# Optimization experiments

Measured on AMD Instinct MI355X. Metric: run time of the kernel, lower is better.

Reference implementation:

```python
import math
import jax, jax.numpy as jnp
import numpy as np

B, T, D, S = 4, 8192, 1024, 32  # batch, seq, dim, num_slots; segment L = T // S


def setup_inputs() -> dict:
    key = jax.random.key(0)
    ks = jax.random.split(key, 11)
    d_inv_sqrt = D ** -0.5
    return {
        "x": jax.random.normal(ks[0], (B, T, D), jnp.float32),
        "gate_w": jax.random.normal(ks[1], (D, D), jnp.float32) * d_inv_sqrt,
        "gate_b": jnp.zeros((D,), jnp.float32),
        "read_q_w": jax.random.normal(ks[2], (D, D), jnp.float32) * 0.02,
        "read_k_w": jax.random.normal(ks[3], (D, D), jnp.float32) * 0.02,
        "read_v_w": jax.random.normal(ks[4], (D, D), jnp.float32) * 0.02,
        "output_w": jax.random.normal(ks[5], (D, D), jnp.float32) * d_inv_sqrt,
        "memory_slots": jax.random.normal(ks[6], (S, D), jnp.float32) * 0.02,
        "write_q_w": jax.random.normal(ks[7], (D, D), jnp.float32) * 0.02,
        "write_k_w": jax.random.normal(ks[8], (D, D), jnp.float32) * 0.02,
        "write_v_w": jax.random.normal(ks[9], (D, D), jnp.float32) * 0.02,
    }


def reference(x, gate_w, gate_b, read_q_w, read_k_w, read_v_w, output_w,
              memory_slots, write_q_w, write_k_w, write_v_w):
    b, t, d = x.shape
    s = memory_slots.shape[0]
    L = t // s  # segment length
    scale = 1.0 / math.sqrt(d)

    h = x @ gate_w.T + gate_b  # [B,T,D] gate pre-activation

    # --- write: per-slot attention over that slot's segment (block-diagonal) ---
    q = memory_slots @ write_q_w.T                      # [S,D]
    xs = x.reshape(b, s, L, d)                          # [B,S,L,D]
    k = xs @ write_k_w.T                                # [B,S,L,D]
    v = xs @ write_v_w.T                                # [B,S,L,D]
    wqk = jnp.einsum('sd,bsld->bsl', q, k) * scale      # [B,S,L]
    wattn = jax.nn.softmax(wqk, axis=-1)
    memory = jnp.einsum('bsl,bsld->bsd', wattn, v)      # [B,S,D]

    # --- read: masked cross-attention from tokens to memory slots ---
    rq = x @ read_q_w.T                                 # [B,T,D]
    rk = memory @ read_k_w.T                            # [B,S,D]
    rv = memory @ read_v_w.T                            # [B,S,D]
    rqk = jnp.einsum('btd,bsd->bts', rq, rk) * scale    # [B,T,S]
    seg = jnp.arange(t) // L                            # token -> segment index
    mask = seg[:, None] <= jnp.arange(s)[None, :]       # [T,S]; attend to slots >= own segment
    rqk = jnp.where(mask[None, :, :], rqk, -jnp.inf)
    rattn = jax.nn.softmax(rqk, axis=-1)
    read = jnp.einsum('bts,bsd->btd', rattn, rv)        # [B,T,D]

    y = x + jax.nn.sigmoid(h) * read
    out = y @ output_w.T
    return out, memory
```

## Files before the change

### kernel.cpp

```cpp
#include <hip/hip_runtime.h>
#include <stdint.h>

#define TB 4
#define TT 8192
#define TD 1024
#define TS 32
#define TL 256
#define BT 32768

typedef unsigned short u16;
typedef __bf16 bf16x8 __attribute__((ext_vector_type(8)));
typedef float f32x4 __attribute__((ext_vector_type(4)));

typedef uint32_t u32_g __attribute__((address_space(1)));
typedef uint32_t u32_l __attribute__((address_space(3)));

#define VMWAIT(N) asm volatile("s_waitcnt vmcnt(" #N ")" ::: "memory")
#define LGKM0()   asm volatile("s_waitcnt lgkmcnt(0)" ::: "memory")

__device__ __forceinline__ u16 f2b(float f){
  union { float f; uint32_t u; } a; a.f = f;
  uint32_t r = a.u + 0x7FFFu + ((a.u >> 16) & 1u);
  return (u16)(r >> 16);
}
__device__ __forceinline__ float b2f(u16 u){
  union { uint32_t u; float f; } a; a.u = ((uint32_t)u) << 16;
  return a.f;
}
__device__ __forceinline__ void gll16(const void* g, void* l){
  __builtin_amdgcn_global_load_lds((const u32_g*)g, (u32_l*)l, 16, 0, 0);
}

__global__ void k_tran(const float* __restrict__ w0, const float* __restrict__ w1,
                       const float* __restrict__ w2, const float* __restrict__ w3,
                       const float* __restrict__ w4, const float* __restrict__ ms,
                       u16* __restrict__ t0, u16* __restrict__ t1,
                       u16* __restrict__ t2, u16* __restrict__ t3,
                       u16* __restrict__ t4, u16* __restrict__ msb){
  int tid = threadIdx.x, z = blockIdx.z;
  if (z == 5){
    int i = (blockIdx.y*16 + blockIdx.x)*256 + tid;
    if (i < 8192){
      float4 v = ((const float4*)ms)[i];
      ushort4 u; u.x=f2b(v.x); u.y=f2b(v.y); u.z=f2b(v.z); u.w=f2b(v.w);
      ((ushort4*)msb)[i] = u;
    }
    return;
  }
  const float* src = (z==0)?w0:(z==1)?w1:(z==2)?w2:(z==3)?w3:w4;
  u16* dst = (z==0)?t0:(z==1)?t1:(z==2)?t2:(z==3)?t3:t4;
  __shared__ float sT[64][65];
  int r0 = blockIdx.y*64, c0 = blockIdx.x*64;
  int lr = tid >> 2, lc = (tid & 3)*16;
  #pragma unroll
  for (int j=0; j<4; ++j){
    float4 v = *(const float4*)(src + (size_t)(r0+lr)*TD + c0 + lc + j*4);
    sT[lr][lc+j*4+0]=v.x; sT[lr][lc+j*4+1]=v.y; sT[lr][lc+j*4+2]=v.z; sT[lr][lc+j*4+3]=v.w;
  }
  __syncthreads();
  int oc = tid >> 2, orh = (tid & 3)*16;
  #pragma unroll
  for (int j=0; j<4; ++j){
    ushort4 u;
    u.x = f2b(sT[orh+j*4+0][oc]);
    u.y = f2b(sT[orh+j*4+1][oc]);
    u.z = f2b(sT[orh+j*4+2][oc]);
    u.w = f2b(sT[orh+j*4+3][oc]);
    *(ushort4*)(dst + (size_t)(c0+oc)*TD + r0 + orh + j*4) = u;
  }
}

__global__ __launch_bounds__(512) void k_smmw(
    const u16* __restrict__ A0, const u16* __restrict__ W0, u16* __restrict__ O0, int tr0, float s0,
    const u16* __restrict__ A1, const u16* __restrict__ W1, u16* __restrict__ O1, int tr1, float s1){
  const u16 *A, *W; u16* O; int tr; float sc;
  if (blockIdx.z == 0){ A=A0; W=W0; O=O0; tr=tr0; sc=s0; }
  else                { A=A1; W=W1; O=O1; tr=tr1; sc=s1; }
  int tid = threadIdx.x, lane = tid & 63, wv = tid >> 6;
  int r15 = lane & 15, kg = lane >> 4;
  int wr = wv >> 2, wc = wv & 3;
  int m0 = blockIdx.y*128 + wr*64;
  int n0 = blockIdx.x*128 + wc*32;
  const u16* ap = A + (size_t)(m0 + r15)*TD + kg*8;
  const u16* bp = W + (size_t)(n0 + r15)*TD + kg*8;
  f32x4 acc[4][2];
  #pragma unroll
  for (int i=0;i<4;i++){ f32x4 z={0,0,0,0}; acc[i][0]=z; acc[i][1]=z; }
  #pragma unroll 2
  for (int k0=0; k0<TD; k0+=32){
    bf16x8 b0 = *(const bf16x8*)(bp + k0);
    bf16x8 b1 = *(const bf16x8*)(bp + 16*TD + k0);
    bf16x8 a0 = *(const bf16x8*)(ap + k0);
    bf16x8 a1 = *(const bf16x8*)(ap + 16*TD + k0);
    bf16x8 a2 = *(const bf16x8*)(ap + 32*TD + k0);
    bf16x8 a3 = *(const bf16x8*)(ap + 48*TD + k0);
    acc[0][0] = __builtin_amdgcn_mfma_f32_16x16x32_bf16(a0, b0, acc[0][0], 0,0,0);
    acc[0][1] = __builtin_amdgcn_mfma_f32_16x16x32_bf16(a0, b1, acc[0][1], 0,0,0);
    acc[1][0] = __builtin_amdgcn_mfma_f32_16x16x32_bf16(a1, b0, acc[1][0], 0,0,0);
    acc[1][1] = __builtin_amdgcn_mfma_f32_16x16x32_bf16(a1, b1, acc[1][1], 0,0,0);
    acc[2][0] = __builtin_amdgcn_mfma_f32_16x16x32_bf16(a2, b0, acc[2][0], 0,0,0);
    acc[2][1] = __builtin_amdgcn_mfma_f32_16x16x32_bf16(a2, b1, acc[2][1], 0,0,0);
    acc[3][0] = __builtin_amdgcn_mfma_f32_16x16x32_bf16(a3, b0, acc[3][0], 0,0,0);
    acc[3][1] = __builtin_amdgcn_mfma_f32_16x16x32_bf16(a3, b1, acc[3][1], 0,0,0);
  }
  #pragma unroll
  for (int mf=0; mf<4; ++mf){
    #pragma unroll
    for (int nf=0; nf<2; ++nf){
      int n = n0 + nf*16 + r15;
      #pragma unroll
      for (int qq=0; qq<4; ++qq){
        float v = acc[mf][nf][qq]*sc;
        int m = m0 + mf*16 + kg*4 + qq;
        if (tr) O[(size_t)n*TD + m] = f2b(v);
        else    O[(size_t)m*TD + n] = f2b(v);
      }
    }
  }
}

__global__ __launch_bounds__(512) void k_qk32(const u16* __restrict__ msb, const u16* __restrict__ WzT,
                                              float* __restrict__ qkp){
  int tid = threadIdx.x, lane = tid & 63, wv = tid >> 6;
  int r15 = lane & 15, kg = lane >> 4;
  int n0 = blockIdx.x*128 + wv*16;
  int kbase = blockIdx.y*512;
  const u16* ap = msb + (size_t)r15*TD + kbase + kg*8;
  const u16* bp = WzT + (size_t)(n0 + r15)*TD + kbase + kg*8;
  f32x4 a0 = {0,0,0,0}, a1 = {0,0,0,0};
  #pragma unroll 4
  for (int k0=0; k0<512; k0+=32){
    bf16x8 b  = *(const bf16x8*)(bp + k0);
    bf16x8 x0 = *(const bf16x8*)(ap + k0);
    bf16x8 x1 = *(const bf16x8*)(ap + 16*TD + k0);
    a0 = __builtin_amdgcn_mfma_f32_16x16x32_bf16(x0, b, a0, 0,0,0);
    a1 = __builtin_amdgcn_mfma_f32_16x16x32_bf16(x1, b, a1, 0,0,0);
  }
  const float sc = 1.0f/32.0f;
  float* o = qkp + (size_t)blockIdx.y*32768;
  #pragma unroll
  for (int qq=0; qq<4; ++qq){
    o[(size_t)(kg*4 + qq)*TD + n0 + r15]      = a0[qq]*sc;
    o[(size_t)(16 + kg*4 + qq)*TD + n0 + r15] = a1[qq]*sc;
  }
}

__global__ void k_convdot(const float* __restrict__ x, const float* __restrict__ qkp,
                          u16* __restrict__ xb, float* __restrict__ wqk,
                          const float* __restrict__ s0, const float* __restrict__ s1,
                          const float* __restrict__ s2, const float* __restrict__ s3,
                          const float* __restrict__ s4,
                          u16* __restrict__ d0, u16* __restrict__ d1,
                          u16* __restrict__ d2, u16* __restrict__ d3,
                          u16* __restrict__ d4){
  int tid = threadIdx.x;
  if (blockIdx.x >= 2048){
    int i = (blockIdx.x - 2048)*256 + tid;
    int mi = i >> 18, j = i & 262143;
    const float* src; u16* dst;
    if      (mi == 0){ src = s0; dst = d0; }
    else if (mi == 1){ src = s1; dst = d1; }
    else if (mi == 2){ src = s2; dst = d2; }
    else if (mi == 3){ src = s3; dst = d3; }
    else             { src = s4; dst = d4; }
    float4 v = ((const float4*)src)[j];
    ushort4 u; u.x=f2b(v.x); u.y=f2b(v.y); u.z=f2b(v.z); u.w=f2b(v.w);
    ((ushort4*)dst)[j] = u;
    return;
  }
  int lane = tid & 63, wv = tid >> 6;
  long bt0 = (long)blockIdx.x * 16;
  int sseg = (int)((bt0 & (TT-1)) >> 8);
  float qv[16];
  #pragma unroll
  for (int i=0;i<4;i++){
    const float* qp = qkp + (size_t)sseg*TD + i*256 + lane*4;
    float4 ta = *(const float4*)qp;
    float4 tb = *(const float4*)(qp + 32768);
    qv[i*4+0]=ta.x+tb.x; qv[i*4+1]=ta.y+tb.y; qv[i*4+2]=ta.z+tb.z; qv[i*4+3]=ta.w+tb.w;
  }
  for (int tok = wv; tok < 16; tok += 4){
    long bt = bt0 + tok;
    const float* xr = x + bt*TD;
    float dot = 0.f;
    #pragma unroll
    for (int i=0;i<4;i++){
      float4 t = *(const float4*)(xr + i*256 + lane*4);
      ushort4 u; u.x=f2b(t.x); u.y=f2b(t.y); u.z=f2b(t.z); u.w=f2b(t.w);
      *(ushort4*)(xb + bt*TD + i*256 + lane*4) = u;
      dot += t.x*qv[i*4] + t.y*qv[i*4+1] + t.z*qv[i*4+2] + t.w*qv[i*4+3];
    }
    #pragma unroll
    for (int o=32;o;o>>=1) dot += __shfl_xor(dot, o);
    if (lane == 0) wqk[bt] = dot;
  }
}

__global__ void k_wattn(const float* __restrict__ wqk, const u16* __restrict__ xb,
                        u16* __restrict__ xbarb){
  __shared__ float sw[TL];
  __shared__ float red[8];
  __shared__ f32x4 part[4][64];
  int tid = threadIdx.x, lane = tid & 63, wv = tid >> 6;
  int b = blockIdx.x >> 5, s = blockIdx.x & 31;
  long base = (long)b*TT + (long)s*TL;
  float v = wqk[base + tid];
  float m = v;
  #pragma unroll
  for (int o=32;o;o>>=1) m = fmaxf(m, __shfl_xor(m, o));
  if (lane == 0) red[wv] = m;
  __syncthreads();
  m = fmaxf(fmaxf(red[0], red[1]), fmaxf(red[2], red[3]));
  float e = __expf(v - m);
  float sm = e;
  #pragma unroll
  for (int o=32;o;o>>=1) sm += __shfl_xor(sm, o);
  if (lane == 0) red[4+wv] = sm;
  __syncthreads();
  sm = red[4]+red[5]+red[6]+red[7];
  sw[tid] = e / sm;
  __syncthreads();
  int d = blockIdx.y*256 + lane*4;
  const u16* xp = xb + (base + wv*64)*TD + d;
  f32x4 acc = {0,0,0,0};
  #pragma unroll 8
  for (int i=0; i<64; ++i){
    float w = sw[wv*64 + i];
    ushort4 u = *(const ushort4*)(xp + (size_t)i*TD);
    acc[0] += w*b2f(u.x); acc[1] += w*b2f(u.y); acc[2] += w*b2f(u.z); acc[3] += w*b2f(u.w);
  }
  part[wv][lane] = acc;
  __syncthreads();
  if (wv == 0){
    f32x4 t0 = part[0][lane], t1 = part[1][lane], t2 = part[2][lane], t3 = part[3][lane];
    ushort4 o;
    o.x = f2b(t0[0]+t1[0]+t2[0]+t3[0]);
    o.y = f2b(t0[1]+t1[1]+t2[1]+t3[1]);
    o.z = f2b(t0[2]+t1[2]+t2[2]+t3[2]);
    o.w = f2b(t0[3]+t1[3]+t2[3]+t3[3]);
    *(ushort4*)(xbarb + ((size_t)b*TS + s)*TD + d) = o;
  }
}

__global__ __launch_bounds__(512) void k_xbar3(const u16* __restrict__ xbarb,
                                               const u16* __restrict__ Wv, const u16* __restrict__ WdT,
                                               const u16* __restrict__ We,
                                               float* __restrict__ memo, u16* __restrict__ rkb,
                                               u16* __restrict__ rvT){
  int z = blockIdx.z;
  const u16* W = (z==0) ? Wv : (z==1) ? WdT : We;
  int tid = threadIdx.x, lane = tid & 63, wv = tid >> 6;
  int r15 = lane & 15, kg = lane >> 4;
  int wr = wv >> 2, wc = wv & 3;
  int n0 = blockIdx.x*128 + wc*32;
  const u16* ap = xbarb + (size_t)(wr*64 + r15)*TD + kg*8;
  const u16* bp = W + (size_t)(n0 + r15)*TD + kg*8;
  f32x4 acc[4][2];
  #pragma unroll
  for (int i=0;i<4;i++){ f32x4 zz={0,0,0,0}; acc[i][0]=zz; acc[i][1]=zz; }
  #pragma unroll 2
  for (int k0=0; k0<TD; k0+=32){
    bf16x8 b0 = *(const bf16x8*)(bp + k0);
    bf16x8 b1 = *(const bf16x8*)(bp + 16*TD + k0);
    bf16x8 a0 = *(const bf16x8*)(ap + k0);
    bf16x8 a1 = *(const bf16x8*)(ap + 16*TD + k0);
    bf16x8 a2 = *(const bf16x8*)(ap + 32*TD + k0);
    bf16x8 a3 = *(const bf16x8*)(ap + 48*TD + k0);
    acc[0][0] = __builtin_amdgcn_mfma_f32_16x16x32_bf16(a0, b0, acc[0][0], 0,0,0);
    acc[0][1] = __builtin_amdgcn_mfma_f32_16x16x32_bf16(a0, b1, acc[0][1], 0,0,0);
    acc[1][0] = __builtin_amdgcn_mfma_f32_16x16x32_bf16(a1, b0, acc[1][0], 0,0,0);
    acc[1][1] = __builtin_amdgcn_mfma_f32_16x16x32_bf16(a1, b1, acc[1][1], 0,0,0);
    acc[2][0] = __builtin_amdgcn_mfma_f32_16x16x32_bf16(a2, b0, acc[2][0], 0,0,0);
    acc[2][1] = __builtin_amdgcn_mfma_f32_16x16x32_bf16(a2, b1, acc[2][1], 0,0,0);
    acc[3][0] = __builtin_amdgcn_mfma_f32_16x16x32_bf16(a3, b0, acc[3][0], 0,0,0);
    acc[3][1] = __builtin_amdgcn_mfma_f32_16x16x32_bf16(a3, b1, acc[3][1], 0,0,0);
  }
  #pragma unroll
  for (int mf=0; mf<4; ++mf){
    #pragma unroll
    for (int nf=0; nf<2; ++nf){
      int n = n0 + nf*16 + r15;
      #pragma unroll
      for (int qq=0; qq<4; ++qq){
        float v = acc[mf][nf][qq];
        int m = wr*64 + mf*16 + kg*4 + qq;
        if (z == 0)      memo[(size_t)m*TD + n] = v;
        else if (z == 1) rkb[(size_t)m*TD + n] = f2b(v);
        else             rvT[((size_t)(m>>5)*TD + n)*TS + (m&31)] = f2b(v);
      }
    }
  }
}

template<bool SIG>
__global__ __launch_bounds__(512, 2) void k_gemm(const u16* __restrict__ A, const u16* __restrict__ Bw,
                                                 const float* __restrict__ bias, void* __restrict__ Cp,
                                                 const u16* __restrict__ rkb, const u16* __restrict__ rvT){
  __shared__ __align__(16) char sL[131072];
  int tid = threadIdx.x, lane = tid & 63, wv = tid >> 6;
  int bid = blockIdx.x;
  int wg = ((bid & 7) << 6) | (bid >> 3);
  int nt = wg & 3, mt = wg >> 2;
  int m0 = mt*256, n0 = nt*256;
  int wr = wv >> 2, wc = wv & 3;
  int r15 = lane & 15, kg = lane >> 4;
  int smin = (m0 & (TT-1)) >> 8;
  bool wcP = SIG && (wc < 2);

  int ard[8], brd[4];
  #pragma unroll
  for (int i=0;i<8;i++){ int row = wr*128 + i*16 + r15; ard[i] = row*128 + ((kg ^ (row&7))<<4); }
  #pragma unroll
  for (int j=0;j<4;j++){ int row = wc*64  + j*16 + r15; brd[j] = row*128 + ((kg ^ (row&7))<<4); }

  const u16* asrc[4]; const u16* bsrc[4]; int ldst[4];
  #pragma unroll
  for (int r=0;r<4;r++){
    int Sp  = r*512 + tid;
    int row = Sp >> 3;
    int kq  = (Sp & 7) ^ (row & 7);
    asrc[r] = A  + (size_t)(m0 + row)*TD + kq*8;
    bsrc[r] = Bw + (size_t)(n0 + row)*TD + kq*8;
    ldst[r] = Sp*16;
  }
  const u16* rkp = rkb + (size_t)((m0 >> 13)*TS + (wc&1)*16 + r15)*TD + kg*8;

  f32x4 acc[8][4];
  #pragma unroll
  for (int i=0;i<8;i++){
    #pragma unroll
    for (int j=0;j<4;j++){ f32x4 z = {0,0,0,0}; acc[i][j] = z; }
  }
  f32x4 pacc[8];
  if constexpr (SIG){
    #pragma unroll
    for (int i=0;i<8;i++){ f32x4 z = {0,0,0,0}; pacc[i] = z; }
  }

  auto stage = [&](int t){
    char* slot = sL + (size_t)(t&1)*65536;
    int k0 = t*64;
    #pragma unroll
    for (int r=0;r<4;r++) gll16(asrc[r] + k0, slot + ldst[r]);
    #pragma unroll
    for (int r=0;r<4;r++) gll16(bsrc[r] + k0, slot + 32768 + ldst[r]);
  };

  auto compute = [&](int t, bf16x8 rk0, bf16x8 rk1){
    const char* sa = sL + (size_t)(t&1)*65536;
    const char* sb = sa + 32768;
    bf16x8 bfg[4], af[4];
    #pragma unroll
    for (int j=0;j<4;j++) bfg[j] = *(const bf16x8*)(sb + brd[j]);
    #pragma unroll
    for (int i=0;i<4;i++) af[i] = *(const bf16x8*)(sa + ard[i]);
    LGKM0();
    __builtin_amdgcn_sched_barrier(0);
    __builtin_amdgcn_s_setprio(1);
    #pragma unroll
    for (int i=0;i<4;i++){
      #pragma unroll
      for (int j=0;j<4;j++)
        acc[i][j] = __builtin_amdgcn_mfma_f32_16x16x32_bf16(af[i], bfg[j], acc[i][j], 0,0,0);
    }
    if constexpr (SIG){
      if (wcP){
        #pragma unroll
        for (int i=0;i<4;i++) pacc[i] = __builtin_amdgcn_mfma_f32_16x16x32_bf16(af[i], rk0, pacc[i], 0,0,0);
      }
    }
    __builtin_amdgcn_s_setprio(0);
    bf16x8 af2[4];
    #pragma unroll
    for (int i=0;i<4;i++) af2[i] = *(const bf16x8*)(sa + (ard[4+i]));
    LGKM0();
    __builtin_amdgcn_sched_barrier(0);
    __builtin_amdgcn_s_setprio(1);
    #pragma unroll
    for (int i=0;i<4;i++){
      #pragma unroll
      for (int j=0;j<4;j++)
        acc[4+i][j] = __builtin_amdgcn_mfma_f32_16x16x32_bf16(af2[i], bfg[j], acc[4+i][j], 0,0,0);
    }
    if constexpr (SIG){
      if (wcP){
        #pragma unroll
        for (int i=0;i<4;i++) pacc[4+i] = __builtin_amdgcn_mfma_f32_16x16x32_bf16(af2[i], rk0, pacc[4+i], 0,0,0);
      }
    }
    __builtin_amdgcn_s_setprio(0);
    bf16x8 bfh[4], ag[4];
    #pragma unroll
    for (int j=0;j<4;j++) bfh[j] = *(const bf16x8*)(sb + (brd[j]^64));
    #pragma unroll
    for (int i=0;i<4;i++) ag[i] = *(const bf16x8*)(sa + (ard[i]^64));
    LGKM0();
    __builtin_amdgcn_sched_barrier(0);
    __builtin_amdgcn_s_setprio(1);
    #pragma unroll
    for (int i=0;i<4;i++){
      #pragma unroll
      for (int j=0;j<4;j++)
        acc[i][j] = __builtin_amdgcn_mfma_f32_16x16x32_bf16(ag[i], bfh[j], acc[i][j], 0,0,0);
    }
    if constexpr (SIG){
      if (wcP){
        #pragma unroll
        for (int i=0;i<4;i++) pacc[i] = __builtin_amdgcn_mfma_f32_16x16x32_bf16(ag[i], rk1, pacc[i], 0,0,0);
      }
    }
    __builtin_amdgcn_s_setprio(0);
    bf16x8 ag2[4];
    #pragma unroll
    for (int i=0;i<4;i++) ag2[i] = *(const bf16x8*)(sa + (ard[4+i]^64));
    LGKM0();
    __builtin_amdgcn_sched_barrier(0);
    __builtin_amdgcn_s_setprio(1);
    #pragma unroll
    for (int i=0;i<4;i++){
      #pragma unroll
      for (int j=0;j<4;j++)
        acc[4+i][j] = __builtin_amdgcn_mfma_f32_16x16x32_bf16(ag2[i], bfh[j], acc[4+i][j], 0,0,0);
    }
    if constexpr (SIG){
      if (wcP){
        #pragma unroll
        for (int i=0;i<4;i++) pacc[4+i] = __builtin_amdgcn_mfma_f32_16x16x32_bf16(ag2[i], rk1, pacc[4+i], 0,0,0);
      }
    }
    __builtin_amdgcn_s_setprio(0);
  };

  stage(0);
  for (int t=0; t<16; ++t){
    if (t > 0) __builtin_amdgcn_s_barrier();
    bf16x8 rk0, rk1;
    if (wcP){
      rk0 = *(const bf16x8*)(rkp + t*64);
      rk1 = *(const bf16x8*)(rkp + t*64 + 32);
      __builtin_amdgcn_sched_barrier(0);
    }
    if (t < 15){
      stage(t+1);
      VMWAIT(8);
    } else {
      VMWAIT(0);
    }
    __builtin_amdgcn_sched_barrier(0);
    __builtin_amdgcn_s_barrier();
    compute(t, rk0, rk1);
  }

  if constexpr (SIG){
    float* Pf = (float*)sL;
    u16* Pb16 = (u16*)(sL + 33792);
    __syncthreads();
    if (wcP){
      #pragma unroll
      for (int i=0;i<8;i++){
        int tok = wr*128 + i*16 + kg*4;
        #pragma unroll
        for (int q=0;q<4;q++)
          Pf[(tok+q)*33 + (wc&1)*16 + r15] = pacc[i][q];
      }
    }
    __syncthreads();
    if (tid < 256){
      float v[32];
      float mx = -1e30f;
      #pragma unroll
      for (int s=0;s<32;s++){
        float t = Pf[tid*33 + s];
        v[s] = t;
        if (s >= smin) mx = fmaxf(mx, t);
      }
      float sum = 0.f;
      #pragma unroll
      for (int s=0;s<32;s++){
        float e = (s >= smin) ? __expf(v[s]-mx) : 0.f;
        v[s] = e; sum += e;
      }
      float rs = 1.f/sum;
      #pragma unroll
      for (int s=0;s<32;s++) Pb16[tid*40 + s] = f2b(v[s]*rs);
    }
    __syncthreads();

    int b = m0 >> 13;
    bf16x8 vfrag[4];
    #pragma unroll
    for (int j=0;j<4;j++){
      int n = n0 + wc*64 + j*16 + r15;
      vfrag[j] = *(const bf16x8*)(rvT + ((size_t)b*TD + n)*TS + kg*8);
    }
    #pragma unroll
    for (int i=0;i<8;i++){
      bf16x8 pfrag = *(const bf16x8*)(Pb16 + (wr*128 + i*16 + r15)*40 + kg*8);
      f32x4 rd[4];
      #pragma unroll
      for (int j=0;j<4;j++){
        f32x4 z = {0,0,0,0};
        rd[j] = __builtin_amdgcn_mfma_f32_16x16x32_bf16(pfrag, vfrag[j], z, 0,0,0);
      }
      int mrow = m0 + wr*128 + i*16 + kg*4;
      #pragma unroll
      for (int j=0;j<4;j++){
        int n = n0 + wc*64 + j*16 + r15;
        float bj = bias[n];
        #pragma unroll
        for (int q=0;q<4;q++){
          float g = 1.f/(1.f + __expf(-(acc[i][j][q] + bj)));
          size_t idx = (size_t)(mrow + q)*TD + n;
          float xv = b2f(A[idx]);
          ((u16*)Cp)[idx] = f2b(xv + g*rd[j][q]);
        }
      }
    }
  } else {
    #pragma unroll
    for (int i=0;i<8;i++){
      int mrow = m0 + wr*128 + i*16 + kg*4;
      #pragma unroll
      for (int j=0;j<4;j++){
        int n = n0 + wc*64 + j*16 + r15;
        #pragma unroll
        for (int q=0;q<4;q++){
          size_t idx = (size_t)(mrow + q)*TD + n;
          ((float*)Cp)[idx] = acc[i][j][q];
        }
      }
    }
  }
}

extern "C" void kernel_launch(void* const* d_in, const int* in_sizes, int n_in,
                              void* d_out, int out_size, void* d_ws, size_t ws_size,
                              hipStream_t stream){
  const float* x   = (const float*)d_in[0];
  const float* gw  = (const float*)d_in[1];
  const float* gb  = (const float*)d_in[2];
  const float* rqw = (const float*)d_in[3];
  const float* rkw = (const float*)d_in[4];
  const float* rvw = (const float*)d_in[5];
  const float* ow  = (const float*)d_in[6];
  const float* ms  = (const float*)d_in[7];
  const float* wqw = (const float*)d_in[8];
  const float* wkw = (const float*)d_in[9];
  const float* wvw = (const float*)d_in[10];
  float* out = (float*)d_out;
  float* mem_out = out + (size_t)BT*TD;

  char* o = (char*)d_out;
  u16* xb    = (u16*)o;
  u16* gwb   = (u16*)(o + 69206016);
  u16* wvwb  = (u16*)(o + 71303168);
  u16* rkwb  = (u16*)(o + 73400320);
  u16* rvwb  = (u16*)(o + 75497472);
  u16* xbarb = (u16*)(o + 79757312);
  u16* rvT   = (u16*)(o + 80281600);
  u16* WvT   = (u16*)(o + 84934656);
  u16* WrqT  = (u16*)(o + 87031808);
  u16* WqT   = (u16*)(o + 89128960);
  u16* WkT   = (u16*)(o + 91226112);
  u16* We    = (u16*)(o + 95420416);
  u16* WdT   = (u16*)(o + 97517568);
  u16* WzT   = (u16*)(o + 99614720);
  u16* msb   = (u16*)(o + 101711872);
  u16* WrkT  = (u16*)(o + 103809024);
  u16* WgT   = (u16*)(o + 105906176);

  char* w = (char*)d_ws;
  u16*   gy    = (u16*)(w);
  float* wqkb  = (float*)(w + 67108864);
  float* qkp   = (float*)(w + 67239936);
  u16*   rkb   = (u16*)(w + 67502080);
  u16*   owb   = (u16*)(w + 68288512);

  k_tran<<<dim3(16,16,6),256,0,stream>>>(wvw, rqw, wqw, wkw, rkw, ms,
                                         WvT, WrqT, WqT, WkT, WrkT, msb);
  k_smmw<<<dim3(8,8,2),512,0,stream>>>(WqT, WkT, WzT, 1, 1.f,
                                       WrkT, WrqT, WgT, 1, 1.f/32.f);
  k_qk32<<<dim3(8,2),512,0,stream>>>(msb, WzT, qkp);
  k_convdot<<<7168,256,0,stream>>>(x, qkp, xb, wqkb,
                                   gw, ow, wvw, rkw, rvw,
                                   gwb, owb, wvwb, rkwb, rvwb);
  k_smmw<<<dim3(8,8,2),512,0,stream>>>(rvwb, WvT, We, 0, 1.f,
                                       WvT, WgT, WdT, 1, 1.f);
  k_wattn<<<dim3(128,4),256,0,stream>>>(wqkb, xb, xbarb);
  k_xbar3<<<dim3(8,1,3),512,0,stream>>>(xbarb, wvwb, WdT, We, mem_out, rkb, rvT);
  k_gemm<true><<<512,512,0,stream>>>(xb, gwb, gb, gy, rkb, rvT);
  k_gemm<false><<<512,512,0,stream>>>(gy, owb, nullptr, d_out, nullptr, nullptr);
}
```

Measured before the change: 399.8 us.

## Merge write-attention and small weight GEMMs into one heterogeneous launch

```diff
diff --git a/kernel.cpp b/kernel.cpp
--- a/kernel.cpp
+++ b/kernel.cpp
@@ -196,49 +196,104 @@
   }
 }
 
-__global__ void k_wattn(const float* __restrict__ wqk, const u16* __restrict__ xb,
-                        u16* __restrict__ xbarb){
-  __shared__ float sw[TL];
-  __shared__ float red[8];
-  __shared__ f32x4 part[4][64];
-  int tid = threadIdx.x, lane = tid & 63, wv = tid >> 6;
-  int b = blockIdx.x >> 5, s = blockIdx.x & 31;
-  long base = (long)b*TT + (long)s*TL;
-  float v = wqk[base + tid];
-  float m = v;
-  #pragma unroll
-  for (int o=32;o;o>>=1) m = fmaxf(m, __shfl_xor(m, o));
-  if (lane == 0) red[wv] = m;
-  __syncthreads();
-  m = fmaxf(fmaxf(red[0], red[1]), fmaxf(red[2], red[3]));
-  float e = __expf(v - m);
-  float sm = e;
-  #pragma unroll
-  for (int o=32;o;o>>=1) sm += __shfl_xor(sm, o);
-  if (lane == 0) red[4+wv] = sm;
-  __syncthreads();
-  sm = red[4]+red[5]+red[6]+red[7];
-  sw[tid] = e / sm;
-  __syncthreads();
-  int d = blockIdx.y*256 + lane*4;
-  const u16* xp = xb + (base + wv*64)*TD + d;
-  f32x4 acc = {0,0,0,0};
-  #pragma unroll 8
-  for (int i=0; i<64; ++i){
-    float w = sw[wv*64 + i];
-    ushort4 u = *(const ushort4*)(xp + (size_t)i*TD);
-    acc[0] += w*b2f(u.x); acc[1] += w*b2f(u.y); acc[2] += w*b2f(u.z); acc[3] += w*b2f(u.w);
-  }
-  part[wv][lane] = acc;
-  __syncthreads();
-  if (wv == 0){
-    f32x4 t0 = part[0][lane], t1 = part[1][lane], t2 = part[2][lane], t3 = part[3][lane];
-    ushort4 o;
-    o.x = f2b(t0[0]+t1[0]+t2[0]+t3[0]);
-    o.y = f2b(t0[1]+t1[1]+t2[1]+t3[1]);
-    o.z = f2b(t0[2]+t1[2]+t2[2]+t3[2]);
-    o.w = f2b(t0[3]+t1[3]+t2[3]+t3[3]);
-    *(ushort4*)(xbarb + ((size_t)b*TS + s)*TD + d) = o;
+__global__ __launch_bounds__(512) void k_wattn_smm(
+    const float* __restrict__ wqk, const u16* __restrict__ xb, u16* __restrict__ xbarb,
+    const u16* __restrict__ A1, const u16* __restrict__ W1, u16* __restrict__ O1,
+    const u16* __restrict__ A2, const u16* __restrict__ W2, u16* __restrict__ O2){
+  __shared__ float sw[2][TL];
+  __shared__ float red[2][8];
+  __shared__ f32x4 part[2][4][64];
+  int tid = threadIdx.x;
+  if (blockIdx.x < 256){
+    int u = tid >> 8;
+    int unit = blockIdx.x*2 + u;
+    int bs = unit >> 2, dch = unit & 3;
+    int b = bs >> 5, s = bs & 31;
+    int t2 = tid & 255, lane = t2 & 63, wv = t2 >> 6;
+    long base = (long)b*TT + (long)s*TL;
+    float v = wqk[base + t2];
+    float m = v;
+    #pragma unroll
+    for (int o=32;o;o>>=1) m = fmaxf(m, __shfl_xor(m, o));
+    if (lane == 0) red[u][wv] = m;
+    __syncthreads();
+    m = fmaxf(fmaxf(red[u][0], red[u][1]), fmaxf(red[u][2], red[u][3]));
+    float e = __expf(v - m);
+    float sm = e;
+    #pragma unroll
+    for (int o=32;o;o>>=1) sm += __shfl_xor(sm, o);
+    if (lane == 0) red[u][4+wv] = sm;
+    __syncthreads();
+    sm = red[u][4]+red[u][5]+red[u][6]+red[u][7];
+    sw[u][t2] = e / sm;
+    __syncthreads();
+    int d = dch*256 + lane*4;
+    const u16* xp = xb + (base + wv*64)*TD + d;
+    f32x4 acc = {0,0,0,0};
+    #pragma unroll 8
+    for (int i=0; i<64; ++i){
+      float w = sw[u][wv*64 + i];
+      ushort4 uu = *(const ushort4*)(xp + (size_t)i*TD);
+      acc[0] += w*b2f(uu.x); acc[1] += w*b2f(uu.y); acc[2] += w*b2f(uu.z); acc[3] += w*b2f(uu.w);
+    }
+    part[u][wv][lane] = acc;
+    __syncthreads();
+    if (wv == 0){
+      f32x4 t0 = part[u][0][lane], t1 = part[u][1][lane], t2v = part[u][2][lane], t3 = part[u][3][lane];
+      ushort4 o;
+      o.x = f2b(t0[0]+t1[0]+t2v[0]+t3[0]);
+      o.y = f2b(t0[1]+t1[1]+t2v[1]+t3[1]);
+      o.z = f2b(t0[2]+t1[2]+t2v[2]+t3[2]);
+      o.w = f2b(t0[3]+t1[3]+t2v[3]+t3[3]);
+      *(ushort4*)(xbarb + ((size_t)b*TS + s)*TD + d) = o;
+    }
+    return;
+  }
+  int bi = blockIdx.x - 256;
+  const u16 *A, *W; u16* O; int tr;
+  if (bi < 64){ A=A1; W=W1; O=O1; tr=0; }
+  else        { A=A2; W=W2; O=O2; tr=1; bi -= 64; }
+  int by = bi >> 3, bx = bi & 7;
+  int lane = tid & 63, wv = tid >> 6;
+  int r15 = lane & 15, kg = lane >> 4;
+  int wr = wv >> 2, wc = wv & 3;
+  int m0 = by*128 + wr*64;
+  int n0 = bx*128 + wc*32;
+  const u16* ap = A + (size_t)(m0 + r15)*TD + kg*8;
+  const u16* bp = W + (size_t)(n0 + r15)*TD + kg*8;
+  f32x4 acc[4][2];
+  #pragma unroll
+  for (int i=0;i<4;i++){ f32x4 z={0,0,0,0}; acc[i][0]=z; acc[i][1]=z; }
+  #pragma unroll 2
+  for (int k0=0; k0<TD; k0+=32){
+    bf16x8 b0 = *(const bf16x8*)(bp + k0);
+    bf16x8 b1 = *(const bf16x8*)(bp + 16*TD + k0);
+    bf16x8 a0 = *(const bf16x8*)(ap + k0);
+    bf16x8 a1 = *(const bf16x8*)(ap + 16*TD + k0);
+    bf16x8 a2 = *(const bf16x8*)(ap + 32*TD + k0);
+    bf16x8 a3 = *(const bf16x8*)(ap + 48*TD + k0);
+    acc[0][0] = __builtin_amdgcn_mfma_f32_16x16x32_bf16(a0, b0, acc[0][0], 0,0,0);
+    acc[0][1] = __builtin_amdgcn_mfma_f32_16x16x32_bf16(a0, b1, acc[0][1], 0,0,0);
+    acc[1][0] = __builtin_amdgcn_mfma_f32_16x16x32_bf16(a1, b0, acc[1][0], 0,0,0);
+    acc[1][1] = __builtin_amdgcn_mfma_f32_16x16x32_bf16(a1, b1, acc[1][1], 0,0,0);
+    acc[2][0] = __builtin_amdgcn_mfma_f32_16x16x32_bf16(a2, b0, acc[2][0], 0,0,0);
+    acc[2][1] = __builtin_amdgcn_mfma_f32_16x16x32_bf16(a2, b1, acc[2][1], 0,0,0);
+    acc[3][0] = __builtin_amdgcn_mfma_f32_16x16x32_bf16(a3, b0, acc[3][0], 0,0,0);
+    acc[3][1] = __builtin_amdgcn_mfma_f32_16x16x32_bf16(a3, b1, acc[3][1], 0,0,0);
+  }
+  #pragma unroll
+  for (int mf=0; mf<4; ++mf){
+    #pragma unroll
+    for (int nf=0; nf<2; ++nf){
+      int n = n0 + nf*16 + r15;
+      #pragma unroll
+      for (int qq=0; qq<4; ++qq){
+        float v = acc[mf][nf][qq];
+        int m = m0 + mf*16 + kg*4 + qq;
+        if (tr) O[(size_t)n*TD + m] = f2b(v);
+        else    O[(size_t)m*TD + n] = f2b(v);
+      }
+    }
   }
 }
 
@@ -305,7 +360,7 @@
   int wr = wv >> 2, wc = wv & 3;
   int r15 = lane & 15, kg = lane >> 4;
   int smin = (m0 & (TT-1)) >> 8;
-  bool wcP = SIG && (wc < 2);
+  bool wcP = SIG && ((wr == 0) ? (wc < 2) : (wc >= 2));
 
   int ard[8], brd[4];
   #pragma unroll
@@ -584,9 +639,9 @@
   k_convdot<<<7168,256,0,stream>>>(x, qkp, xb, wqkb,
                                    gw, ow, wvw, rkw, rvw,
                                    gwb, owb, wvwb, rkwb, rvwb);
-  k_smmw<<<dim3(8,8,2),512,0,stream>>>(rvwb, WvT, We, 0, 1.f,
-                                       WvT, WgT, WdT, 1, 1.f);
-  k_wattn<<<dim3(128,4),256,0,stream>>>(wqkb, xb, xbarb);
+  k_wattn_smm<<<384,512,0,stream>>>(wqkb, xb, xbarb,
+                                    rvwb, WvT, We,
+                                    WvT, WgT, WdT);
   k_xbar3<<<dim3(8,1,3),512,0,stream>>>(xbarb, wvwb, WdT, We, mem_out, rkb, rvT);
   k_gemm<true><<<512,512,0,stream>>>(xb, gwb, gb, gy, rkb, rvT);
   k_gemm<false><<<512,512,0,stream>>>(gy, owb, nullptr, d_out, nullptr, nullptr);
```

Result: faster. 388.8 us (median of 2 runs) (-2.8%).
